# Kernel optimization log

Measured on AMD Instinct MI355X. Metric: run time of the kernel, lower is better.

The kernel has to match this reference:

```python
import jax, jax.numpy as jnp
import numpy as np

N_NODES = 100000
D_GRAPH = 512    # graph_embedding_dim
D_ROUTE = 1024   # routes_embedding_dim
N_ROUTES = 16384
ROUTE_LEN = 32
N_BLOCKS = 3


def setup_inputs() -> dict:
    key = jax.random.key(0)
    ks = jax.random.split(key, 2 + 2 * N_BLOCKS)
    graph_embedding = jax.random.normal(ks[0], (N_NODES, D_GRAPH), dtype=jnp.float32)
    locations_idx = jax.random.randint(ks[1], (N_ROUTES, ROUTE_LEN), 0, N_NODES, dtype=jnp.int64)
    # Linear block chain: first block D_GRAPH->D_ROUTE, rest D_ROUTE->D_ROUTE, ReLU each
    dims = [D_GRAPH] + [D_ROUTE] * N_BLOCKS
    inp = {"graph_embedding": graph_embedding, "locations_idx": locations_idx}
    for i in range(N_BLOCKS):
        fan_in = dims[i]
        scale = 1.0 / np.sqrt(fan_in)
        inp[f"W{i}"] = jax.random.uniform(ks[2 + 2 * i], (fan_in, dims[i + 1]), jnp.float32, -scale, scale)
        inp[f"b{i}"] = jax.random.uniform(ks[3 + 2 * i], (dims[i + 1],), jnp.float32, -scale, scale)
    return inp


def reference(graph_embedding, locations_idx, W0, b0, W1, b1, W2, b2):
    # per-route gather: [R, L, D] then max over route positions -> [R, D]
    gathered = graph_embedding[locations_idx]          # [n_routes, route_len, d_graph]
    routes_emb = jnp.max(gathered, axis=1)             # [n_routes, d_graph]
    # linear block chain (Linear + ReLU per block)
    x = jax.nn.relu(routes_emb @ W0 + b0)
    x = jax.nn.relu(x @ W1 + b1)
    x = jax.nn.relu(x @ W2 + b2)
    return x
```

## Files before the change

### kernel.cpp

```cpp
#include <hip/hip_runtime.h>
#include <hip/hip_bf16.h>
#include <cstdint>


typedef __attribute__((ext_vector_type(8))) short          bf16x8;
typedef __attribute__((ext_vector_type(8))) unsigned short u16x8;
typedef __attribute__((ext_vector_type(4))) float          f32x4;

__device__ __forceinline__ unsigned short f2b_rne(float f) {
    union { float f; uint32_t i; } x; x.f = f;
    uint32_t lsb = (x.i >> 16) & 1u;
    return (unsigned short)((x.i + 0x7fffu + lsb) >> 16);
}
__device__ __forceinline__ float b2f(unsigned short u) {
    union { float f; uint32_t i; } x; x.i = ((uint32_t)u) << 16; return x.f;
}

__device__ __forceinline__ void async_copy16(const void* gptr, void* lptr) {
    __builtin_amdgcn_global_load_lds(
        (const __attribute__((address_space(1))) unsigned int*)gptr,
        (__attribute__((address_space(3))) unsigned int*)lptr, 16, 0, 0);
}

__global__ __launch_bounds__(256)
void convert_f32_bf16(const float* __restrict__ in, unsigned short* __restrict__ out)
{
    const size_t i = ((size_t)blockIdx.x * 256 + threadIdx.x) * 8;
    const float4* p = reinterpret_cast<const float4*>(in + i);
    float4 v0 = p[0], v1 = p[1];
    u16x8 o;
    o[0] = f2b_rne(v0.x); o[1] = f2b_rne(v0.y); o[2] = f2b_rne(v0.z); o[3] = f2b_rne(v0.w);
    o[4] = f2b_rne(v1.x); o[5] = f2b_rne(v1.y); o[6] = f2b_rne(v1.z); o[7] = f2b_rne(v1.w);
    *reinterpret_cast<u16x8*>(out + i) = o;
}

__global__ void transpose_f32_bf16(const float* __restrict__ W,
                                   unsigned short* __restrict__ Wt,
                                   int K, int N)
{
    __shared__ float tile[32][33];
    const int n0 = blockIdx.x * 32;
    const int k0 = blockIdx.y * 32;
    const int tx = threadIdx.x & 31;
    const int ty = threadIdx.x >> 5;
#pragma unroll
    for (int i = 0; i < 32; i += 8)
        tile[ty + i][tx] = W[(size_t)(k0 + ty + i) * N + (n0 + tx)];
    __syncthreads();
#pragma unroll
    for (int i = 0; i < 32; i += 8)
        Wt[(size_t)(n0 + ty + i) * K + (k0 + tx)] = f2b_rne(tile[tx][ty + i]);
}

__global__ void gather_max_bf16(const unsigned short* __restrict__ graphb,
                                const int* __restrict__ idx32,
                                unsigned short* __restrict__ routes)
{
    bool is64 = true;
#pragma unroll
    for (int k = 0; k < 64; k++) is64 &= (idx32[2 * k + 1] == 0);
    const int stride = is64 ? 64 : 32;
    const int step   = is64 ? 2  : 1;

    const int wave  = threadIdx.x >> 6;
    const int lane  = threadIdx.x & 63;
    const int route = (blockIdx.x * 4 + wave) * 4;
    const int col   = lane * 8;

    float m[4][8];
#pragma unroll
    for (int t = 0; t < 4; t++)
#pragma unroll
        for (int j = 0; j < 8; j++) m[t][j] = -INFINITY;

    const int* ip = idx32 + (size_t)route * stride;
#pragma unroll 2
    for (int l = 0; l < 32; l++) {
        u16x8 v[4];
#pragma unroll
        for (int t = 0; t < 4; t++) {
            const int node = ip[t * stride + l * step];
            v[t] = *reinterpret_cast<const u16x8*>(graphb + (size_t)node * 512 + col);
        }
#pragma unroll
        for (int t = 0; t < 4; t++)
#pragma unroll
            for (int j = 0; j < 8; j++)
                m[t][j] = fmaxf(m[t][j], b2f(v[t][j]));
    }
#pragma unroll
    for (int t = 0; t < 4; t++) {
        u16x8 o;
#pragma unroll
        for (int j = 0; j < 8; j++) {
            union { float f; uint32_t i; } x; x.f = m[t][j];
            o[j] = (unsigned short)(x.i >> 16);
        }
        *reinterpret_cast<u16x8*>(routes + (size_t)(route + t) * 512 + col) = o;
    }
}

__global__ void gather_max_f32(const float* __restrict__ graph,
                               const int* __restrict__ idx32,
                               unsigned short* __restrict__ routes)
{
    bool is64 = true;
#pragma unroll
    for (int k = 0; k < 64; k++) is64 &= (idx32[2 * k + 1] == 0);
    const int stride = is64 ? 64 : 32;
    const int step   = is64 ? 2  : 1;

    const int wave  = threadIdx.x >> 6;
    const int lane  = threadIdx.x & 63;
    const int route = (blockIdx.x * 4 + wave) * 2;
    const int col   = lane * 8;

    float m0[8], m1[8];
#pragma unroll
    for (int j = 0; j < 8; j++) { m0[j] = -INFINITY; m1[j] = -INFINITY; }

    const int* ip0 = idx32 + (size_t)route * stride;
    const int* ip1 = ip0 + stride;
#pragma unroll 4
    for (int l = 0; l < 32; l++) {
        const int n0 = ip0[l * step];
        const int n1 = ip1[l * step];
        const float4* p0 = reinterpret_cast<const float4*>(graph + (size_t)n0 * 512 + col);
        const float4* p1 = reinterpret_cast<const float4*>(graph + (size_t)n1 * 512 + col);
        float4 a0 = p0[0], a1 = p0[1];
        float4 b0 = p1[0], b1 = p1[1];
        m0[0] = fmaxf(m0[0], a0.x); m0[1] = fmaxf(m0[1], a0.y);
        m0[2] = fmaxf(m0[2], a0.z); m0[3] = fmaxf(m0[3], a0.w);
        m0[4] = fmaxf(m0[4], a1.x); m0[5] = fmaxf(m0[5], a1.y);
        m0[6] = fmaxf(m0[6], a1.z); m0[7] = fmaxf(m0[7], a1.w);
        m1[0] = fmaxf(m1[0], b0.x); m1[1] = fmaxf(m1[1], b0.y);
        m1[2] = fmaxf(m1[2], b0.z); m1[3] = fmaxf(m1[3], b0.w);
        m1[4] = fmaxf(m1[4], b1.x); m1[5] = fmaxf(m1[5], b1.y);
        m1[6] = fmaxf(m1[6], b1.z); m1[7] = fmaxf(m1[7], b1.w);
    }
    u16x8 o0, o1;
#pragma unroll
    for (int j = 0; j < 8; j++) { o0[j] = f2b_rne(m0[j]); o1[j] = f2b_rne(m1[j]); }
    *reinterpret_cast<u16x8*>(routes + (size_t)route * 512 + col)       = o0;
    *reinterpret_cast<u16x8*>(routes + (size_t)(route + 1) * 512 + col) = o1;
}

template <int K, typename OutT>
__global__ __launch_bounds__(512, 2)
void gemm_bt_relu_8p(const unsigned short* __restrict__ A,
                     const unsigned short* __restrict__ Bt,
                     const float* __restrict__ bias,
                     OutT* __restrict__ C)
{
    constexpr int N  = 1024;
    constexpr int BK = 32;
    constexpr int NT = K / BK;

    __shared__ __align__(16) unsigned short As[4][256 * BK];
    __shared__ __align__(16) unsigned short Bs[4][256 * BK];

    const int tid  = threadIdx.x;
    const int wave = tid >> 6;
    const int lane = tid & 63;
    const int quad = lane >> 4;
    const int l16  = lane & 15;
    const int wm   = (wave >> 2) * 128;
    const int wn   = (wave & 3) * 64;

    const int swz = (blockIdx.x & 7) * 32 + (blockIdx.x >> 3);
    const int bm  = (swz >> 2) * 256;
    const int bn  = (swz & 3) * 256;

    const unsigned short* ag[2];
    const unsigned short* bg[2];
    int ao[2];
#pragma unroll
    for (int j = 0; j < 2; j++) {
        const int s = j * 512 + tid;
        const int r = s >> 2;
        const int c = (s & 3) ^ ((r >> 1) & 3);
        ag[j] = A  + (size_t)(bm + r) * K + c * 8;
        bg[j] = Bt + (size_t)(bn + r) * K + c * 8;
        ao[j] = s * 8;
    }

#pragma unroll
    for (int t = 0; t < 3; t++) {
#pragma unroll
        for (int j = 0; j < 2; j++) async_copy16(ag[j] + t * BK, &As[t][ao[j]]);
#pragma unroll
        for (int j = 0; j < 2; j++) async_copy16(bg[j] + t * BK, &Bs[t][ao[j]]);
    }
    asm volatile("s_waitcnt vmcnt(8)" ::: "memory");
    __builtin_amdgcn_s_barrier();

    f32x4 acc[8][4] = {};

    for (int t = 0; t < NT; ++t) {
        const unsigned short* Ab = As[t & 3];
        const unsigned short* Bb = Bs[t & 3];

        bf16x8 bf[4], a0[4];
#pragma unroll
        for (int i = 0; i < 4; i++) {
            const int row = wn + i * 16 + l16;
            bf[i] = *reinterpret_cast<const bf16x8*>(
                Bb + row * BK + ((quad ^ ((row >> 1) & 3)) << 3));
        }
#pragma unroll
        for (int i = 0; i < 4; i++) {
            const int row = wm + i * 16 + l16;
            a0[i] = *reinterpret_cast<const bf16x8*>(
                Ab + row * BK + ((quad ^ ((row >> 1) & 3)) << 3));
        }
        if (t + 3 < NT) {
            const int tb = (t + 3) & 3;
            const int k0 = (t + 3) * BK;
#pragma unroll
            for (int j = 0; j < 2; j++) async_copy16(ag[j] + k0, &As[tb][ao[j]]);
        }
        __builtin_amdgcn_s_barrier();
        __builtin_amdgcn_s_setprio(1);
#pragma unroll
        for (int mi = 0; mi < 4; mi++)
#pragma unroll
            for (int ni = 0; ni < 4; ni++)
                acc[mi][ni] = __builtin_amdgcn_mfma_f32_16x16x32_bf16(
                    a0[mi], bf[ni], acc[mi][ni], 0, 0, 0);
        __builtin_amdgcn_s_setprio(0);
        __builtin_amdgcn_s_barrier();

        bf16x8 a1[4];
#pragma unroll
        for (int i = 0; i < 4; i++) {
            const int row = wm + 64 + i * 16 + l16;
            a1[i] = *reinterpret_cast<const bf16x8*>(
                Ab + row * BK + ((quad ^ ((row >> 1) & 3)) << 3));
        }
        if (t + 3 < NT) {
            const int tb = (t + 3) & 3;
            const int k0 = (t + 3) * BK;
#pragma unroll
            for (int j = 0; j < 2; j++) async_copy16(bg[j] + k0, &Bs[tb][ao[j]]);
        }
        __builtin_amdgcn_s_barrier();
        __builtin_amdgcn_s_setprio(1);
#pragma unroll
        for (int mi = 0; mi < 4; mi++)
#pragma unroll
            for (int ni = 0; ni < 4; ni++)
                acc[mi + 4][ni] = __builtin_amdgcn_mfma_f32_16x16x32_bf16(
                    a1[mi], bf[ni], acc[mi + 4][ni], 0, 0, 0);
        __builtin_amdgcn_s_setprio(0);
        if (t + 3 < NT)      asm volatile("s_waitcnt vmcnt(8)" ::: "memory");
        else if (t + 2 < NT) asm volatile("s_waitcnt vmcnt(4)" ::: "memory");
        else                 asm volatile("s_waitcnt vmcnt(0)" ::: "memory");
        __builtin_amdgcn_s_barrier();
    }

#pragma unroll
    for (int ni = 0; ni < 4; ni++) {
        const int n  = bn + wn + ni * 16 + l16;
        const float bv = bias[n];
#pragma unroll
        for (int mi = 0; mi < 8; mi++) {
            const int mbase = bm + wm + mi * 16 + quad * 4;
#pragma unroll
            for (int r = 0; r < 4; r++) {
                float v = fmaxf(acc[mi][ni][r] + bv, 0.0f);
                if constexpr (sizeof(OutT) == 2)
                    C[(size_t)(mbase + r) * N + n] = (OutT)f2b_rne(v);
                else
                    C[(size_t)(mbase + r) * N + n] = (OutT)v;
            }
        }
    }
}

extern "C" void kernel_launch(void* const* d_in, const int* in_sizes, int n_in,
                              void* d_out, int out_size, void* d_ws, size_t ws_size,
                              hipStream_t stream)
{
    constexpr int N_ROUTES = 16384;
    constexpr int N_NODES  = 100000;
    constexpr int D_GRAPH  = 512;
    constexpr int D_ROUTE  = 1024;

    const float* graph = (const float*)d_in[0];
    const int*   idx   = (const int*)d_in[1];
    const float* W0    = (const float*)d_in[2];
    const float* b0    = (const float*)d_in[3];
    const float* W1    = (const float*)d_in[4];
    const float* b1    = (const float*)d_in[5];
    const float* W2    = (const float*)d_in[6];
    const float* b2    = (const float*)d_in[7];
    float*       out   = (float*)d_out;

    char* w = (char*)d_ws;
    unsigned short* Wt0    = (unsigned short*)w; w += (size_t)D_ROUTE * D_GRAPH * 2;
    unsigned short* Wt1    = (unsigned short*)w; w += (size_t)D_ROUTE * D_ROUTE * 2;
    unsigned short* Wt2    = (unsigned short*)w; w += (size_t)D_ROUTE * D_ROUTE * 2;
    unsigned short* routes = (unsigned short*)w; w += (size_t)N_ROUTES * D_GRAPH * 2;
    unsigned short* x1     = (unsigned short*)w; w += (size_t)N_ROUTES * D_ROUTE * 2;
    unsigned short* x2     = (unsigned short*)w; w += (size_t)N_ROUTES * D_ROUTE * 2;
    unsigned short* graphb = (unsigned short*)w;
    const size_t need_bf16 = (size_t)(w - (char*)d_ws) + (size_t)N_NODES * D_GRAPH * 2;
    const bool   use_bf16  = (ws_size >= need_bf16);

    transpose_f32_bf16<<<dim3(D_ROUTE / 32, D_GRAPH / 32), 256, 0, stream>>>(W0, Wt0, D_GRAPH, D_ROUTE);
    transpose_f32_bf16<<<dim3(D_ROUTE / 32, D_ROUTE / 32), 256, 0, stream>>>(W1, Wt1, D_ROUTE, D_ROUTE);
    transpose_f32_bf16<<<dim3(D_ROUTE / 32, D_ROUTE / 32), 256, 0, stream>>>(W2, Wt2, D_ROUTE, D_ROUTE);

    if (use_bf16) {
        convert_f32_bf16<<<(N_NODES * D_GRAPH / 8) / 256, 256, 0, stream>>>(graph, graphb);
        gather_max_bf16<<<N_ROUTES / 16, 256, 0, stream>>>(graphb, idx, routes);
    } else {
        gather_max_f32<<<N_ROUTES / 8, 256, 0, stream>>>(graph, idx, routes);
    }

    gemm_bt_relu_8p<512,  unsigned short><<<256, 512, 0, stream>>>(routes, Wt0, b0, x1);
    gemm_bt_relu_8p<1024, unsigned short><<<256, 512, 0, stream>>>(x1, Wt1, b1, x2);
    gemm_bt_relu_8p<1024, float><<<256, 512, 0, stream>>>(x2, Wt2, b2, out);
}
```

Measured before the change: 528.6 us.

## Merge weight transposes and graph conversion into one prep launch; stage route indices in LDS

Combines the three weight-transpose kernels and the graph fp32-to-bf16 conversion into a single prep kernel whose blocks dispatch on block index, cutting launch count and letting the small transposes overlap with the large conversion. The bf16 gather kernel now loads each block's 16x32 route indices into shared memory once and reads node ids from LDS instead of global memory, with a deeper unroll of the route loop. This costs an extra barrier and some LDS per block, and adds register pressure from the larger unroll.

Result: faster. 513.0 us (-3.0%).

```diff
diff --git a/kernel.cpp b/kernel.cpp
--- a/kernel.cpp
+++ b/kernel.cpp
@@ -23,24 +23,33 @@
 }
 
 __global__ __launch_bounds__(256)
-void convert_f32_bf16(const float* __restrict__ in, unsigned short* __restrict__ out)
-{
-    const size_t i = ((size_t)blockIdx.x * 256 + threadIdx.x) * 8;
-    const float4* p = reinterpret_cast<const float4*>(in + i);
-    float4 v0 = p[0], v1 = p[1];
-    u16x8 o;
-    o[0] = f2b_rne(v0.x); o[1] = f2b_rne(v0.y); o[2] = f2b_rne(v0.z); o[3] = f2b_rne(v0.w);
-    o[4] = f2b_rne(v1.x); o[5] = f2b_rne(v1.y); o[6] = f2b_rne(v1.z); o[7] = f2b_rne(v1.w);
-    *reinterpret_cast<u16x8*>(out + i) = o;
-}
-
-__global__ void transpose_f32_bf16(const float* __restrict__ W,
-                                   unsigned short* __restrict__ Wt,
-                                   int K, int N)
+void prep(int conv_blocks,
+          const float* __restrict__ graph, unsigned short* __restrict__ graphb,
+          const float* __restrict__ W0, unsigned short* __restrict__ Wt0,
+          const float* __restrict__ W1, unsigned short* __restrict__ Wt1,
+          const float* __restrict__ W2, unsigned short* __restrict__ Wt2)
 {
     __shared__ float tile[32][33];
-    const int n0 = blockIdx.x * 32;
-    const int k0 = blockIdx.y * 32;
+
+    if ((int)blockIdx.x < conv_blocks) {
+        const size_t i = ((size_t)blockIdx.x * 256 + threadIdx.x) * 8;
+        const float4* p = reinterpret_cast<const float4*>(graph + i);
+        float4 v0 = p[0], v1 = p[1];
+        u16x8 o;
+        o[0] = f2b_rne(v0.x); o[1] = f2b_rne(v0.y); o[2] = f2b_rne(v0.z); o[3] = f2b_rne(v0.w);
+        o[4] = f2b_rne(v1.x); o[5] = f2b_rne(v1.y); o[6] = f2b_rne(v1.z); o[7] = f2b_rne(v1.w);
+        *reinterpret_cast<u16x8*>(graphb + i) = o;
+        return;
+    }
+
+    int b = blockIdx.x - conv_blocks;
+    const float* W; unsigned short* Wt; int K;
+    if (b < 512)       { W = W0; Wt = Wt0; K = 512;  }
+    else if (b < 1536) { b -= 512;  W = W1; Wt = Wt1; K = 1024; }
+    else               { b -= 1536; W = W2; Wt = Wt2; K = 1024; }
+    constexpr int N = 1024;
+    const int n0 = (b & 31) * 32;
+    const int k0 = (b >> 5) * 32;
     const int tx = threadIdx.x & 31;
     const int ty = threadIdx.x >> 5;
 #pragma unroll
@@ -52,20 +61,30 @@
         Wt[(size_t)(n0 + ty + i) * K + (k0 + tx)] = f2b_rne(tile[tx][ty + i]);
 }
 
-__global__ void gather_max_bf16(const unsigned short* __restrict__ graphb,
-                                const int* __restrict__ idx32,
-                                unsigned short* __restrict__ routes)
-{
+__global__ __launch_bounds__(256)
+void gather_max_bf16(const unsigned short* __restrict__ graphb,
+                     const int* __restrict__ idx32,
+                     unsigned short* __restrict__ routes)
+{
+    __shared__ int sidx[16][32];
+
     bool is64 = true;
 #pragma unroll
     for (int k = 0; k < 64; k++) is64 &= (idx32[2 * k + 1] == 0);
     const int stride = is64 ? 64 : 32;
     const int step   = is64 ? 2  : 1;
 
-    const int wave  = threadIdx.x >> 6;
-    const int lane  = threadIdx.x & 63;
-    const int route = (blockIdx.x * 4 + wave) * 4;
-    const int col   = lane * 8;
+    const int route0 = blockIdx.x * 16;
+    for (int e = threadIdx.x; e < 512; e += 256) {
+        const int r = e >> 5, l = e & 31;
+        sidx[r][l] = idx32[(size_t)(route0 + r) * stride + l * step];
+    }
+    __syncthreads();
+
+    const int wave = threadIdx.x >> 6;
+    const int lane = threadIdx.x & 63;
+    const int rl   = wave * 4;
+    const int col  = lane * 8;
 
     float m[4][8];
 #pragma unroll
@@ -73,13 +92,12 @@
 #pragma unroll
         for (int j = 0; j < 8; j++) m[t][j] = -INFINITY;
 
-    const int* ip = idx32 + (size_t)route * stride;
-#pragma unroll 2
+#pragma unroll 4
     for (int l = 0; l < 32; l++) {
         u16x8 v[4];
 #pragma unroll
         for (int t = 0; t < 4; t++) {
-            const int node = ip[t * stride + l * step];
+            const int node = sidx[rl + t][l];
             v[t] = *reinterpret_cast<const u16x8*>(graphb + (size_t)node * 512 + col);
         }
 #pragma unroll
@@ -96,7 +114,7 @@
             union { float f; uint32_t i; } x; x.f = m[t][j];
             o[j] = (unsigned short)(x.i >> 16);
         }
-        *reinterpret_cast<u16x8*>(routes + (size_t)(route + t) * 512 + col) = o;
+        *reinterpret_cast<u16x8*>(routes + (size_t)(route0 + rl + t) * 512 + col) = o;
     }
 }
 
@@ -307,12 +325,14 @@
     const size_t need_bf16 = (size_t)(w - (char*)d_ws) + (size_t)N_NODES * D_GRAPH * 2;
     const bool   use_bf16  = (ws_size >= need_bf16);
 
-    transpose_f32_bf16<<<dim3(D_ROUTE / 32, D_GRAPH / 32), 256, 0, stream>>>(W0, Wt0, D_GRAPH, D_ROUTE);
-    transpose_f32_bf16<<<dim3(D_ROUTE / 32, D_ROUTE / 32), 256, 0, stream>>>(W1, Wt1, D_ROUTE, D_ROUTE);
-    transpose_f32_bf16<<<dim3(D_ROUTE / 32, D_ROUTE / 32), 256, 0, stream>>>(W2, Wt2, D_ROUTE, D_ROUTE);
+    constexpr int CONV_BLOCKS = (N_NODES * D_GRAPH / 8) / 256;
+    constexpr int TR_BLOCKS   = 512 + 1024 + 1024;
+
+    const int conv_blocks = use_bf16 ? CONV_BLOCKS : 0;
+    prep<<<conv_blocks + TR_BLOCKS, 256, 0, stream>>>(
+        conv_blocks, graph, graphb, W0, Wt0, W1, Wt1, W2, Wt2);
 
     if (use_bf16) {
-        convert_f32_bf16<<<(N_NODES * D_GRAPH / 8) / 256, 256, 0, stream>>>(graph, graphb);
         gather_max_bf16<<<N_ROUTES / 16, 256, 0, stream>>>(graphb, idx, routes);
     } else {
         gather_max_f32<<<N_ROUTES / 8, 256, 0, stream>>>(graph, idx, routes);
```
